# Kernel tuning notes

Measured on AMD Instinct MI355X. Metric: run time of the kernel, lower is better.

Reference implementation:

```python
import jax, jax.numpy as jnp
import numpy as np

B, N, HID, H = 16, 256, 512, 8
DK = HID // H          # att_size = 64
FEAT = 8               # storage/operator feature dim
MLP_H = 64             # interaction MLP hidden dim
LAM = 0.1              # htap_lambda
SCALE = DK ** -0.5


def _pair_bias(feat, W1, b1, W2, b2):
    """MLP([v_i || v_j || |v_i - v_j|]) for all pairs -> [B,N,N,H].
    Split W1 over the three concat blocks so the per-node parts are O(N)."""
    F = feat.shape[-1]
    Wa, Wb, Wc = W1[:F], W1[F:2 * F], W1[2 * F:]
    hi = feat @ Wa                                    # [B,N,MLP_H]
    hj = feat @ Wb                                    # [B,N,MLP_H]
    diff = jnp.abs(feat[:, :, None, :] - feat[:, None, :, :])  # [B,N,N,F]
    h = jax.nn.relu(hi[:, :, None, :] + hj[:, None, :, :] + diff @ Wc + b1)
    return h @ W2 + b2                                # [B,N,N,H]


def setup_inputs() -> dict:
    key = jax.random.key(0)
    ks = jax.random.split(key, 24)
    g = lambda i, shape, s=0.05: jax.random.normal(ks[i], shape, jnp.float32) * (1.0 if s is None else 1.0) * (s / 0.05 * 0.05 if False else 1.0)
    def w(i, shape, scale):
        return jax.random.normal(ks[i], shape, jnp.float32) * scale
    inp = {
        "q": w(0, (B, N, HID), 1.0),
        "k": w(1, (B, N, HID), 1.0),
        "v": w(2, (B, N, HID), 1.0),
        "tree_attn_bias": w(3, (B, H, N, N), 1.0),
        "storage_features": w(4, (B, N, FEAT), 1.0),
        "operator_features": w(5, (B, N, FEAT), 1.0),
        # attention projections (stored as [in,out])
        "Wq": w(6, (HID, HID), HID ** -0.5), "bq": jnp.zeros((HID,), jnp.float32),
        "Wk": w(7, (HID, HID), HID ** -0.5), "bk": jnp.zeros((HID,), jnp.float32),
        "Wv": w(8, (HID, HID), HID ** -0.5), "bv": jnp.zeros((HID,), jnp.float32),
        "Wo": w(9, (HID, HID), HID ** -0.5), "bo": jnp.zeros((HID,), jnp.float32),
        # f_s interaction MLP: Linear(3*FEAT,64) -> ReLU -> Linear(64,H)
        "fs_W1": w(10, (3 * FEAT, MLP_H), (3 * FEAT) ** -0.5), "fs_b1": jnp.zeros((MLP_H,), jnp.float32),
        "fs_W2": w(11, (MLP_H, H), MLP_H ** -0.5), "fs_b2": jnp.zeros((H,), jnp.float32),
        # f_o interaction MLP
        "fo_W1": w(12, (3 * FEAT, MLP_H), (3 * FEAT) ** -0.5), "fo_b1": jnp.zeros((MLP_H,), jnp.float32),
        "fo_W2": w(13, (MLP_H, H), MLP_H ** -0.5), "fo_b2": jnp.zeros((H,), jnp.float32),
    }
    return inp


def reference(q, k, v, tree_attn_bias, storage_features, operator_features,
              Wq, bq, Wk, bk, Wv, bv, Wo, bo,
              fs_W1, fs_b1, fs_W2, fs_b2, fo_W1, fo_b1, fo_W2, fo_b2):
    # projections -> [B,H,N,DK]
    qh = (q @ Wq + bq).reshape(B, N, H, DK).transpose(0, 2, 1, 3) * SCALE
    kh = (k @ Wk + bk).reshape(B, N, H, DK).transpose(0, 2, 1, 3)
    vh = (v @ Wv + bv).reshape(B, N, H, DK).transpose(0, 2, 1, 3)

    scores = jnp.einsum("bhnd,bhmd->bhnm", qh, kh) + tree_attn_bias

    htap = (_pair_bias(storage_features, fs_W1, fs_b1, fs_W2, fs_b2)
            + _pair_bias(operator_features, fo_W1, fo_b1, fo_W2, fo_b2))  # [B,N,N,H]
    scores = scores + LAM * htap.transpose(0, 3, 1, 2)

    attn = jax.nn.softmax(scores, axis=-1)            # dropout rate 0 (eval)
    x = jnp.einsum("bhnm,bhmd->bhnd", attn, vh)
    x = x.transpose(0, 2, 1, 3).reshape(B, N, HID)
    return x @ Wo + bo
```

## Files before the change

kernel.cpp:

```cpp
#include <hip/hip_runtime.h>
#include <hip/hip_bf16.h>
#include <stdint.h>

#define B_    16
#define N_    256
#define HID_  512
#define H_    8
#define DK_   64
#define FEAT_ 8
#define MLPH_ 64
#define LAM_  0.1f
#define SCALE_ 0.125f

typedef short bf16x8 __attribute__((ext_vector_type(8)));
typedef float f32x4  __attribute__((ext_vector_type(4)));

union U8 { uint4 u; bf16x8 h; ushort s[8]; };

__device__ __forceinline__ uint16_t f32_to_bf16(float x) {
    uint32_t u = __float_as_uint(x);
    u += 0x7fffu + ((u >> 16) & 1u);
    return (uint16_t)(u >> 16);
}
__device__ __forceinline__ float bf16_to_f32(uint16_t v) {
    return __uint_as_float(((uint32_t)v) << 16);
}
__device__ __forceinline__ uint32_t pk_bf16(float lo, float hi) {
    float2 xy; xy.x = lo; xy.y = hi;
    __hip_bfloat162 b2 = __float22bfloat162_rn(xy);
    return *(uint32_t*)&b2;
}
#define LDS_FENCE() asm volatile("s_waitcnt lgkmcnt(0)" ::: "memory")

__global__ __launch_bounds__(256, 4) void proj_kernel(
    const float* __restrict__ q, const float* __restrict__ k, const float* __restrict__ v,
    const float* __restrict__ Wq, const float* __restrict__ bq,
    const float* __restrict__ Wk, const float* __restrict__ bk,
    const float* __restrict__ Wv, const float* __restrict__ bv,
    ushort* __restrict__ qh, ushort* __restrict__ kh, ushort* __restrict__ vh)
{
    int z = blockIdx.z;
    const float* X    = (z == 0) ? q  : (z == 1) ? k  : v;
    const float* W    = (z == 0) ? Wq : (z == 1) ? Wk : Wv;
    const float* bias = (z == 0) ? bq : (z == 1) ? bk : bv;
    ushort* out       = (z == 0) ? qh : (z == 1) ? kh : vh;
    float scale       = (z == 0) ? SCALE_ : 1.0f;

    int m0 = blockIdx.x * 128;
    int h  = blockIdx.y;
    int c0 = h * 64;

    __shared__ __align__(16) ushort Xs[2][128 * 40];
    __shared__ __align__(16) ushort Ws[2][64 * 40];

    int t = threadIdx.x;
    int wave = t >> 6, lane = t & 63;
    int l15 = lane & 15, qd = lane >> 4;

    int xr = t >> 1, xc = (t & 1) * 16;
    int kr = t & 15, nq = t >> 4;

    f32x4 acc0[4] = {}, acc1[4] = {};

    float4 xv[4], w0, w1;
    #pragma unroll
    for (int p = 0; p < 4; p++)
        xv[p] = *(const float4*)&X[(m0 + xr) * HID_ + xc + p * 4];
    w0 = *(const float4*)&W[(2 * kr) * HID_ + c0 + nq * 4];
    w1 = *(const float4*)&W[(2 * kr + 1) * HID_ + c0 + nq * 4];

    for (int k0 = 0; k0 < HID_; k0 += 32) {
        int buf = (k0 >> 5) & 1;
        #pragma unroll
        for (int p = 0; p < 4; p++) {
            ushort4 o;
            o.x = f32_to_bf16(xv[p].x); o.y = f32_to_bf16(xv[p].y);
            o.z = f32_to_bf16(xv[p].z); o.w = f32_to_bf16(xv[p].w);
            *(ushort4*)&Xs[buf][xr * 40 + xc + p * 4] = o;
        }
        {
            const float* a0 = &w0.x; const float* a1 = &w1.x;
            #pragma unroll
            for (int i = 0; i < 4; i++) {
                uint32_t pk = (uint32_t)f32_to_bf16(a0[i]) | ((uint32_t)f32_to_bf16(a1[i]) << 16);
                *(uint32_t*)&Ws[buf][(nq * 4 + i) * 40 + 2 * kr] = pk;
            }
        }
        __syncthreads();

        if (k0 + 32 < HID_) {
            int kn = k0 + 32;
            #pragma unroll
            for (int p = 0; p < 4; p++)
                xv[p] = *(const float4*)&X[(m0 + xr) * HID_ + kn + xc + p * 4];
            w0 = *(const float4*)&W[(kn + 2 * kr) * HID_ + c0 + nq * 4];
            w1 = *(const float4*)&W[(kn + 2 * kr + 1) * HID_ + c0 + nq * 4];
        }

        bf16x8 af0 = *(const bf16x8*)&Xs[buf][(wave * 32 + l15) * 40 + qd * 8];
        bf16x8 af1 = *(const bf16x8*)&Xs[buf][(wave * 32 + 16 + l15) * 40 + qd * 8];
        #pragma unroll
        for (int nt = 0; nt < 4; nt++) {
            bf16x8 bf = *(const bf16x8*)&Ws[buf][(nt * 16 + l15) * 40 + qd * 8];
            acc0[nt] = __builtin_amdgcn_mfma_f32_16x16x32_bf16(af0, bf, acc0[nt], 0, 0, 0);
            acc1[nt] = __builtin_amdgcn_mfma_f32_16x16x32_bf16(af1, bf, acc1[nt], 0, 0, 0);
        }
    }

    #pragma unroll
    for (int nt = 0; nt < 4; nt++) {
        float bb = bias[c0 + nt * 16 + l15];
        #pragma unroll
        for (int g = 0; g < 2; g++) {
            const f32x4& a = g ? acc1[nt] : acc0[nt];
            #pragma unroll
            for (int r = 0; r < 4; r++) {
                int m = m0 + wave * 32 + g * 16 + qd * 4 + r;
                int b_ = m >> 8, n_ = m & 255;
                float val = (a[r] + bb) * scale;
                out[(((b_ * H_ + h) * N_) + n_) * DK_ + nt * 16 + l15] = f32_to_bf16(val);
            }
        }
    }
}

__global__ void prep_frags(const float* __restrict__ fsW1, const float* __restrict__ foW1,
                           const float* __restrict__ fsW2, const float* __restrict__ foW2,
                           uint4* __restrict__ bfrag1, uint4* __restrict__ bfrag2)
{
    int t = threadIdx.x;
    #pragma unroll
    for (int e = t; e < 512; e += 256) {
        int nt = e >> 6, lane = e & 63, l15 = lane & 15, qd = lane >> 4;
        int n = nt * 16 + l15;
        ushort vals[8];
        #pragma unroll
        for (int u = 0; u < 8; u++) {
            float x = 0.f;
            if (n < 64) {
                if (qd == 0) x = fsW1[(16 + u) * 64 + n];
                else if (qd == 1) x = fsW1[(8 + u) * 64 + n];
            } else {
                int n2 = n - 64;
                if (qd == 2) x = foW1[(16 + u) * 64 + n2];
                else if (qd == 3) x = foW1[(8 + u) * 64 + n2];
            }
            vals[u] = f32_to_bf16(x);
        }
        uint4 pk;
        pk.x = (uint32_t)vals[0] | ((uint32_t)vals[1] << 16);
        pk.y = (uint32_t)vals[2] | ((uint32_t)vals[3] << 16);
        pk.z = (uint32_t)vals[4] | ((uint32_t)vals[5] << 16);
        pk.w = (uint32_t)vals[6] | ((uint32_t)vals[7] << 16);
        bfrag1[e] = pk;
    }
    {
        int e = t;
        int ks = e >> 6, lane = e & 63, l15 = lane & 15, qd = lane >> 4;
        ushort vals[8];
        #pragma unroll
        for (int u = 0; u < 8; u++) {
            float x = 0.f;
            if (l15 < 8) {
                int k2 = ks * 32 + qd * 8 + u;
                int c = ((k2 & 7) << 4) | (k2 >> 3);
                x = LAM_ * ((c < 64) ? fsW2[c * 8 + l15] : foW2[(c - 64) * 8 + l15]);
            }
            vals[u] = f32_to_bf16(x);
        }
        uint4 pk;
        pk.x = (uint32_t)vals[0] | ((uint32_t)vals[1] << 16);
        pk.y = (uint32_t)vals[2] | ((uint32_t)vals[3] << 16);
        pk.z = (uint32_t)vals[4] | ((uint32_t)vals[5] << 16);
        pk.w = (uint32_t)vals[6] | ((uint32_t)vals[7] << 16);
        bfrag2[e] = pk;
    }
}

#define HSTRIDE 136
__global__ __launch_bounds__(256, 3) void pair_bias_mfma(
    const float* __restrict__ sf, const float* __restrict__ of,
    const float* __restrict__ fsW1, const float* __restrict__ fsb1,
    const float* __restrict__ foW1, const float* __restrict__ fob1,
    const float* __restrict__ fsb2, const float* __restrict__ fob2,
    const uint4* __restrict__ bfrag1, const uint4* __restrict__ bfrag2,
    ushort* __restrict__ mlpb)
{
    __shared__ __align__(16) ushort hbuf[4][2][16 * HSTRIDE];
    __shared__ float hisbuf[128];
    __shared__ __align__(4) ushort tbuf[4][2][8 * 16];

    int i = blockIdx.x, b = blockIdx.y;
    int t = threadIdx.x;
    int wave = t >> 6, lane = t & 63;
    int l15 = lane & 15, qd = lane >> 4;

    if (t < 128) {
        int set = t >> 6, kk = t & 63;
        const float* W1 = set ? foW1 : fsW1;
        const float* fi = (set ? of : sf) + (b * N_ + i) * FEAT_;
        float a = (set ? fob1 : fsb1)[kk];
        #pragma unroll
        for (int f = 0; f < FEAT_; f++) a += fi[f] * W1[f * 64 + kk];
        hisbuf[t] = a;
    }

    bf16x8 Bf1[8], Bf2[4];
    #pragma unroll
    for (int nt = 0; nt < 8; nt++) { U8 u; u.u = bfrag1[nt * 64 + lane]; Bf1[nt] = u.h; }
    #pragma unroll
    for (int ks = 0; ks < 4; ks++) { U8 u; u.u = bfrag2[ks * 64 + lane]; Bf2[ks] = u.h; }

    const float* fsr = sf + (b * N_ + i) * FEAT_;
    const float* forr = of + (b * N_ + i) * FEAT_;
    float fsi[8], foi[8];
    #pragma unroll
    for (int u = 0; u < 8; u++) { fsi[u] = fsr[u]; foi[u] = forr[u]; }
    float b2l = LAM_ * (fsb2[l15 & 7] + fob2[l15 & 7]);

    bf16x8 af[4];
    #pragma unroll
    for (int qt = 0; qt < 4; qt++) {
        int j = (wave * 4 + qt) * 16 + l15;
        const float* fr = ((qd < 2) ? sf : of) + (b * N_ + j) * FEAT_;
        float4 f0 = *(const float4*)&fr[0];
        float4 f1 = *(const float4*)&fr[4];
        float vals[8] = {f0.x, f0.y, f0.z, f0.w, f1.x, f1.y, f1.z, f1.w};
        if ((qd & 1) == 0) {
            const float* fi = (qd < 2) ? fsi : foi;
            #pragma unroll
            for (int u = 0; u < 8; u++) vals[u] = fabsf(vals[u] - fi[u]);
        }
        U8 au;
        #pragma unroll
        for (int p = 0; p < 4; p++)
            ((uint32_t*)&au)[p] = pk_bf16(vals[2 * p], vals[2 * p + 1]);
        af[qt] = au.h;
    }

    __syncthreads();
    float hv[8];
    #pragma unroll
    for (int nt = 0; nt < 8; nt++) hv[nt] = hisbuf[nt * 16 + l15];

    {
        f32x4 S1[8];
        #pragma unroll
        for (int nt = 0; nt < 8; nt++) {
            f32x4 c0 = {hv[nt], hv[nt], hv[nt], hv[nt]};
            S1[nt] = __builtin_amdgcn_mfma_f32_16x16x32_bf16(af[0], Bf1[nt], c0, 0, 0, 0);
        }
        ushort* hb = &hbuf[wave][0][0];
        #pragma unroll
        for (int r = 0; r < 4; r++) {
            uint4 w;
            w.x = pk_bf16(fmaxf(S1[0][r], 0.f), fmaxf(S1[1][r], 0.f));
            w.y = pk_bf16(fmaxf(S1[2][r], 0.f), fmaxf(S1[3][r], 0.f));
            w.z = pk_bf16(fmaxf(S1[4][r], 0.f), fmaxf(S1[5][r], 0.f));
            w.w = pk_bf16(fmaxf(S1[6][r], 0.f), fmaxf(S1[7][r], 0.f));
            *(uint4*)&hb[(qd * 4 + r) * HSTRIDE + l15 * 8] = w;
        }
    }

    #pragma unroll
    for (int qt = 0; qt < 4; qt++) {
        ushort* hbC = &hbuf[wave][qt & 1][0];
        ushort* hbN = &hbuf[wave][(qt & 1) ^ 1][0];
        LDS_FENCE();

        f32x4 Sn[8];
        if (qt < 3) {
            #pragma unroll
            for (int nt = 0; nt < 8; nt++) {
                f32x4 c0 = {hv[nt], hv[nt], hv[nt], hv[nt]};
                Sn[nt] = __builtin_amdgcn_mfma_f32_16x16x32_bf16(af[qt + 1], Bf1[nt], c0, 0, 0, 0);
            }
        }

        f32x4 S2 = {b2l, b2l, b2l, b2l};
        #pragma unroll
        for (int ks = 0; ks < 4; ks++) {
            bf16x8 a2 = *(const bf16x8*)&hbC[l15 * HSTRIDE + ks * 32 + qd * 8];
            S2 = __builtin_amdgcn_mfma_f32_16x16x32_bf16(a2, Bf2[ks], S2, 0, 0, 0);
        }

        ushort* tb = &tbuf[wave][qt & 1][0];
        if (l15 < 8) {
            #pragma unroll
            for (int r = 0; r < 4; r++)
                tb[l15 * 16 + qd * 4 + r] = f32_to_bf16(S2[r]);
        }
        LDS_FENCE();

        {
            int j0 = (wave * 4 + qt) * 16;
            int h2 = lane >> 3, jp = lane & 7;
            uint32_t lo = tb[h2 * 16 + jp * 2];
            uint32_t hi = tb[h2 * 16 + jp * 2 + 1];
            uint32_t pk = lo | (hi << 16);
            *(uint32_t*)&mlpb[(((size_t)(b * H_ + h2) * N_ + i) * N_) + j0 + jp * 2] = pk;
        }

        if (qt < 3) {
            #pragma unroll
            for (int r = 0; r < 4; r++) {
                uint4 w;
                w.x = pk_bf16(fmaxf(Sn[0][r], 0.f), fmaxf(Sn[1][r], 0.f));
                w.y = pk_bf16(fmaxf(Sn[2][r], 0.f), fmaxf(Sn[3][r], 0.f));
                w.z = pk_bf16(fmaxf(Sn[4][r], 0.f), fmaxf(Sn[5][r], 0.f));
                w.w = pk_bf16(fmaxf(Sn[6][r], 0.f), fmaxf(Sn[7][r], 0.f));
                *(uint4*)&hbN[(qd * 4 + r) * HSTRIDE + l15 * 8] = w;
            }
        }
    }
}

__global__ __launch_bounds__(256, 2) void attn_kernel(
    const ushort* __restrict__ qh, const ushort* __restrict__ kh,
    const ushort* __restrict__ vh, const float* __restrict__ tree,
    const ushort* __restrict__ mlpb, ushort* __restrict__ ctxb)
{
    __shared__ __align__(16) ushort bufKP[256 * 72];
    __shared__ __align__(16) ushort bufV[64 * 264];

    int blk = blockIdx.x;
    int bh = blk >> 2;
    int quarter = blk & 3;

    int t = threadIdx.x;
    int wave = t >> 6, lane = t & 63;
    int l15 = lane & 15, qd = lane >> 4;
    int i0w = quarter * 64 + wave * 16;

    const ushort* khb = kh + (size_t)bh * N_ * DK_;
    const ushort* vhb = vh + (size_t)bh * N_ * DK_;

    #pragma unroll
    for (int u = t; u < 2048; u += 256) {
        int j = u >> 3, seg = (u & 7) * 8;
        uint4 kv = *(const uint4*)&khb[j * DK_ + seg];
        *(uint4*)&bufKP[j * 72 + seg] = kv;
    }
    #pragma unroll
    for (int u = t; u < 1024; u += 256) {
        int rp = u & 127, d0 = (u >> 7) * 8;
        U8 v0, v1;
        v0.u = *(const uint4*)&vhb[(2 * rp) * DK_ + d0];
        v1.u = *(const uint4*)&vhb[(2 * rp + 1) * DK_ + d0];
        #pragma unroll
        for (int jj = 0; jj < 8; jj++) {
            uint32_t pk = (uint32_t)v0.s[jj] | ((uint32_t)v1.s[jj] << 16);
            *(uint32_t*)&bufV[(d0 + jj) * 264 + 2 * rp] = pk;
        }
    }
    __syncthreads();

    bf16x8 a0, a1;
    {
        size_t qb = ((size_t)bh * N_ + i0w + l15) * DK_;
        U8 t0, t1;
        t0.u = *(const uint4*)&qh[qb + qd * 8];
        t1.u = *(const uint4*)&qh[qb + 32 + qd * 8];
        a0 = t0.h; a1 = t1.h;
    }
    f32x4 S[16];
    #pragma unroll
    for (int nt = 0; nt < 16; nt++) {
        f32x4 acc = {};
        bf16x8 b0 = *(const bf16x8*)&bufKP[(nt * 16 + l15) * 72 + qd * 8];
        bf16x8 b1 = *(const bf16x8*)&bufKP[(nt * 16 + l15) * 72 + 32 + qd * 8];
        acc = __builtin_amdgcn_mfma_f32_16x16x32_bf16(a0, b0, acc, 0, 0, 0);
        acc = __builtin_amdgcn_mfma_f32_16x16x32_bf16(a1, b1, acc, 0, 0, 0);
        S[nt] = acc;
    }

    {
        size_t base = ((size_t)bh * N_ + i0w + qd * 4) * N_ + l15;
        const float*  tr = tree + base;
        const ushort* mb = mlpb + base;
        #pragma unroll
        for (int nt = 0; nt < 16; nt++)
            #pragma unroll
            for (int r = 0; r < 4; r++)
                S[nt][r] += tr[(size_t)r * N_ + nt * 16] + bf16_to_f32(mb[(size_t)r * N_ + nt * 16]);
    }

    float mx[4], sm[4];
    #pragma unroll
    for (int r = 0; r < 4; r++) mx[r] = -1e30f;
    #pragma unroll
    for (int nt = 0; nt < 16; nt++)
        #pragma unroll
        for (int r = 0; r < 4; r++) mx[r] = fmaxf(mx[r], S[nt][r]);
    #pragma unroll
    for (int r = 0; r < 4; r++) {
        #pragma unroll
        for (int m = 1; m <= 8; m <<= 1) mx[r] = fmaxf(mx[r], __shfl_xor(mx[r], m));
    }
    #pragma unroll
    for (int r = 0; r < 4; r++) sm[r] = 0.f;
    #pragma unroll
    for (int nt = 0; nt < 16; nt++)
        #pragma unroll
        for (int r = 0; r < 4; r++) {
            float e = __expf(S[nt][r] - mx[r]);
            S[nt][r] = e;
            sm[r] += e;
        }
    #pragma unroll
    for (int r = 0; r < 4; r++) {
        #pragma unroll
        for (int m = 1; m <= 8; m <<= 1) sm[r] += __shfl_xor(sm[r], m);
        sm[r] = 1.0f / sm[r];
    }

    __syncthreads();

    {
        uint32_t* Pw = (uint32_t*)&bufKP[wave * 16 * 264];
        #pragma unroll
        for (int nt = 0; nt < 16; nt++)
            #pragma unroll
            for (int r = 0; r < 4; r++) {
                float p = S[nt][r] * sm[r];
                float po = __shfl_xor(p, 1);
                uint32_t pk = (uint32_t)f32_to_bf16(p) | ((uint32_t)f32_to_bf16(po) << 16);
                if ((lane & 1) == 0)
                    Pw[(qd * 4 + r) * 132 + nt * 8 + (l15 >> 1)] = pk;
            }
    }
    __syncthreads();

    const ushort* Pw = &bufKP[wave * 16 * 264];
    f32x4 O[4] = {};
    #pragma unroll
    for (int ks = 0; ks < 8; ks++) {
        int j0 = ks * 32;
        bf16x8 pa = *(const bf16x8*)&Pw[l15 * 264 + j0 + qd * 8];
        #pragma unroll
        for (int ntd = 0; ntd < 4; ntd++) {
            bf16x8 vb = *(const bf16x8*)&bufV[(ntd * 16 + l15) * 264 + j0 + qd * 8];
            O[ntd] = __builtin_amdgcn_mfma_f32_16x16x32_bf16(pa, vb, O[ntd], 0, 0, 0);
        }
    }

    #pragma unroll
    for (int ntd = 0; ntd < 4; ntd++)
        #pragma unroll
        for (int r = 0; r < 4; r++)
            ctxb[((size_t)bh * N_ + i0w + qd * 4 + r) * DK_ + ntd * 16 + l15] =
                f32_to_bf16(O[ntd][r]);
}

__global__ __launch_bounds__(256, 4) void outproj_kernel(
    const ushort* __restrict__ ctxb, const float* __restrict__ Wo,
    const float* __restrict__ bo, float* __restrict__ out)
{
    int m0 = blockIdx.x * 64;
    int c0 = blockIdx.y * 64;

    __shared__ __align__(16) ushort Xs[64 * 40];
    __shared__ __align__(16) ushort Ws[64 * 40];

    int t = threadIdx.x;
    int wave = t >> 6, lane = t & 63;
    int l15 = lane & 15, qd = lane >> 4;

    f32x4 acc[4] = {};

    for (int k0 = 0; k0 < HID_; k0 += 32) {
        __syncthreads();
        {
            int r = t >> 2, s8 = (t & 3) * 8;
            int m = m0 + r, b_ = m >> 8, n_ = m & 255;
            uint4 xv = *(const uint4*)&ctxb[(((b_ * H_ + (k0 >> 6)) * N_) + n_) * DK_ + (k0 & 63) + s8];
            *(uint4*)&Xs[r * 40 + s8] = xv;
        }
        {
            int kr = t & 15, nq = t >> 4;
            float4 w0 = *(const float4*)&Wo[(k0 + 2 * kr) * HID_ + c0 + nq * 4];
            float4 w1 = *(const float4*)&Wo[(k0 + 2 * kr + 1) * HID_ + c0 + nq * 4];
            const float* a0 = &w0.x; const float* a1 = &w1.x;
            #pragma unroll
            for (int i = 0; i < 4; i++) {
                uint32_t pk = (uint32_t)f32_to_bf16(a0[i]) | ((uint32_t)f32_to_bf16(a1[i]) << 16);
                *(uint32_t*)&Ws[(nq * 4 + i) * 40 + 2 * kr] = pk;
            }
        }
        __syncthreads();
        bf16x8 af = *(const bf16x8*)&Xs[(wave * 16 + l15) * 40 + qd * 8];
        #pragma unroll
        for (int nt = 0; nt < 4; nt++) {
            bf16x8 bf = *(const bf16x8*)&Ws[(nt * 16 + l15) * 40 + qd * 8];
            acc[nt] = __builtin_amdgcn_mfma_f32_16x16x32_bf16(af, bf, acc[nt], 0, 0, 0);
        }
    }

    #pragma unroll
    for (int nt = 0; nt < 4; nt++) {
        float bb = bo[c0 + nt * 16 + l15];
        #pragma unroll
        for (int r = 0; r < 4; r++) {
            int m = m0 + wave * 16 + qd * 4 + r;
            out[m * HID_ + c0 + nt * 16 + l15] = acc[nt][r] + bb;
        }
    }
}

extern "C" void kernel_launch(void* const* d_in, const int* in_sizes, int n_in,
                              void* d_out, int out_size, void* d_ws, size_t ws_size,
                              hipStream_t stream)
{
    const float* q    = (const float*)d_in[0];
    const float* k    = (const float*)d_in[1];
    const float* v    = (const float*)d_in[2];
    const float* tree = (const float*)d_in[3];
    const float* sf   = (const float*)d_in[4];
    const float* of   = (const float*)d_in[5];
    const float* Wq   = (const float*)d_in[6];
    const float* bq   = (const float*)d_in[7];
    const float* Wk   = (const float*)d_in[8];
    const float* bk   = (const float*)d_in[9];
    const float* Wv   = (const float*)d_in[10];
    const float* bv   = (const float*)d_in[11];
    const float* Wo   = (const float*)d_in[12];
    const float* bo   = (const float*)d_in[13];
    const float* fsW1 = (const float*)d_in[14];
    const float* fsb1 = (const float*)d_in[15];
    const float* fsW2 = (const float*)d_in[16];
    const float* fsb2 = (const float*)d_in[17];
    const float* foW1 = (const float*)d_in[18];
    const float* fob1 = (const float*)d_in[19];
    const float* foW2 = (const float*)d_in[20];
    const float* fob2 = (const float*)d_in[21];

    char* ws = (char*)d_ws;
    ushort* qh     = (ushort*)(ws + 0);
    ushort* kh     = (ushort*)(ws + 4194304);
    ushort* vh     = (ushort*)(ws + 8388608);
    ushort* ctxb   = (ushort*)(ws + 12582912);
    uint4*  bfrag1 = (uint4*)(ws + 16777216);
    uint4*  bfrag2 = (uint4*)(ws + 16785408);
    ushort* mlpb   = (ushort*)(ws + 23080960);

    proj_kernel<<<dim3(32, 8, 3), 256, 0, stream>>>(q, k, v, Wq, bq, Wk, bk, Wv, bv, qh, kh, vh);
    prep_frags<<<1, 256, 0, stream>>>(fsW1, foW1, fsW2, foW2, bfrag1, bfrag2);
    pair_bias_mfma<<<dim3(N_, B_), 256, 0, stream>>>(sf, of, fsW1, fsb1, foW1, fob1,
                                                     fsb2, fob2, bfrag1, bfrag2, mlpb);
    attn_kernel<<<512, 256, 0, stream>>>(qh, kh, vh, tree, mlpb, ctxb);
    outproj_kernel<<<dim3(64, 8), 256, 0, stream>>>(ctxb, Wo, bo, (float*)d_out);
}
```

Before: 225.3 us.

## Store MLP bias in MFMA-friendly layout and stage tree bias through LDS

The pair-bias MLP kernel now writes its bf16 output in a permuted layout so the attention kernel can fetch each lane's 16 bias values with two 16-byte vector loads instead of 64 scalar strided loads. The tree bias is loaded with coalesced float4 reads into per-wave LDS scratch (reusing the K buffer after a barrier) and then read back in the MFMA fragment order. This targets uncoalesced global loads in the bias-add phase. The cost is an extra __syncthreads, LDS traffic, and scattered 2-byte stores on the write side.

```diff
diff --git a/kernel.cpp b/kernel.cpp
--- a/kernel.cpp
+++ b/kernel.cpp
@@ -293,12 +293,11 @@
         LDS_FENCE();
 
         {
-            int j0 = (wave * 4 + qt) * 16;
+            int j0q = wave * 4 + qt;
             int h2 = lane >> 3, jp = lane & 7;
-            uint32_t lo = tb[h2 * 16 + jp * 2];
-            uint32_t hi = tb[h2 * 16 + jp * 2 + 1];
-            uint32_t pk = lo | (hi << 16);
-            *(uint32_t*)&mlpb[(((size_t)(b * H_ + h2) * N_ + i) * N_) + j0 + jp * 2] = pk;
+            size_t base = (((size_t)(b * H_ + h2) * N_ + i) * 16 + jp * 2) * 16 + j0q;
+            mlpb[base]      = tb[h2 * 16 + jp * 2];
+            mlpb[base + 16] = tb[h2 * 16 + jp * 2 + 1];
         }
 
         if (qt < 3) {
@@ -374,15 +373,44 @@
         S[nt] = acc;
     }
 
+    __syncthreads();
+
     {
-        size_t base = ((size_t)bh * N_ + i0w + qd * 4) * N_ + l15;
-        const float*  tr = tree + base;
-        const ushort* mb = mlpb + base;
-        #pragma unroll
-        for (int nt = 0; nt < 16; nt++)
-            #pragma unroll
-            for (int r = 0; r < 4; r++)
-                S[nt][r] += tr[(size_t)r * N_ + nt * 16] + bf16_to_f32(mb[(size_t)r * N_ + nt * 16]);
+        size_t rbase = (((size_t)bh * N_ + i0w + qd * 4) * 16 + l15) * 16;
+        #pragma unroll
+        for (int r = 0; r < 4; r++) {
+            const ushort* mbp = mlpb + rbase + (size_t)r * 256;
+            U8 ma, mb2;
+            ma.u  = *(const uint4*)&mbp[0];
+            mb2.u = *(const uint4*)&mbp[8];
+            #pragma unroll
+            for (int nt = 0; nt < 8; nt++) S[nt][r]     += bf16_to_f32(ma.s[nt]);
+            #pragma unroll
+            for (int nt = 0; nt < 8; nt++) S[nt + 8][r] += bf16_to_f32(mb2.s[nt]);
+        }
+    }
+
+    {
+        float* tls = (float*)&bufKP[wave * 4608];
+        #pragma unroll
+        for (int half = 0; half < 2; half++) {
+            #pragma unroll
+            for (int f = 0; f < 8; f++) {
+                int L = f * 64 + lane;
+                int row = L >> 5, c4 = L & 31;
+                float4 tv = *(const float4*)
+                    &tree[((size_t)bh * N_ + i0w + row) * N_ + half * 128 + c4 * 4];
+                *(float4*)&tls[row * 132 + c4 * 4] = tv;
+            }
+            LDS_FENCE();
+            #pragma unroll
+            for (int nt = 0; nt < 8; nt++) {
+                #pragma unroll
+                for (int r = 0; r < 4; r++)
+                    S[half * 8 + nt][r] += tls[(qd * 4 + r) * 132 + nt * 16 + l15];
+            }
+            LDS_FENCE();
+        }
     }
 
     float mx[4], sm[4];
```

Result: slower. 246.9 us (+9.6%).
